# Kernel tuning notes

Hardware: AMD Instinct MI355X
Metric: run time of the kernel (lower is better)

Reference implementation:

```python
import jax, jax.numpy as jnp
import numpy as np

B, S, D = 4, 2048, 768

def setup_inputs() -> dict:
    key = jax.random.key(0)
    ks = jax.random.split(key, 7)
    scale = 1.0 / np.sqrt(D)
    x = jax.random.normal(ks[0], (B, S, D), dtype=jnp.float32)
    Wq = jax.random.uniform(ks[1], (D, D), jnp.float32, -scale, scale)
    bq = jax.random.uniform(ks[2], (D,), jnp.float32, -scale, scale)
    Wk = jax.random.uniform(ks[3], (D, D), jnp.float32, -scale, scale)
    bk = jax.random.uniform(ks[4], (D,), jnp.float32, -scale, scale)
    Wv = jax.random.uniform(ks[5], (D, D), jnp.float32, -scale, scale)
    bv = jax.random.uniform(ks[6], (D,), jnp.float32, -scale, scale)
    return {"x": x, "Wq": Wq, "bq": bq, "Wk": Wk, "bk": bk, "Wv": Wv, "bv": bv}

def reference(x, Wq, bq, Wk, bk, Wv, bv):
    d = x.shape[-1]
    q = jnp.einsum('bsd,de->bse', x, Wq) + bq
    k = jnp.einsum('bsd,de->bse', x, Wk) + bk
    v = jnp.einsum('bsd,de->bse', x, Wv) + bv
    scores = jnp.einsum('bqd,bkd->bqk', q, k) / jnp.sqrt(jnp.asarray(d, x.dtype))
    attn = jax.nn.softmax(scores, axis=-1)  # [B,S,S]
    return jnp.einsum('bqk,bkd->bqd', attn, v)
```

## Files before the change

kernel.cpp:

```cpp
#include <hip/hip_runtime.h>
#include <hip/hip_bf16.h>


typedef __attribute__((ext_vector_type(8))) short short8;
typedef __attribute__((ext_vector_type(4))) short short4v;
typedef __attribute__((ext_vector_type(4))) float float4v;

static constexpr int B_ = 4, S_ = 2048, D_ = 768;
static constexpr int MS = B_ * S_;

__device__ inline short f2bf(float f) {
  __hip_bfloat16 h = __float2bfloat16(f);
  union { __hip_bfloat16 h; short s; } u; u.h = h; return u.s;
}
__device__ inline float bf2f(short s) {
  union { unsigned int u; float f; } c;
  c.u = ((unsigned int)(unsigned short)s) << 16; return c.f;
}

typedef const __attribute__((address_space(1))) unsigned int g_u32;
typedef __attribute__((address_space(3))) unsigned int l_u32;

__device__ __forceinline__ void glds16(const short* g, short* l) {
  __builtin_amdgcn_global_load_lds((g_u32*)g, (l_u32*)l, 16, 0, 0);
}

__global__ __launch_bounds__(256)
void cast_f32_bf16(const float* __restrict__ x, short* __restrict__ y, int n) {
  int i = (blockIdx.x * 256 + threadIdx.x) * 4;
  if (i + 3 < n) {
    float4v v = *(const float4v*)(x + i);
    short4v o;
    o.x = f2bf(v.x); o.y = f2bf(v.y); o.z = f2bf(v.z); o.w = f2bf(v.w);
    *(short4v*)(y + i) = o;
  }
}

__global__ void transpose_cast_w(const float* __restrict__ W0, const float* __restrict__ W1,
                                 const float* __restrict__ W2,
                                 short* __restrict__ T0, short* __restrict__ T1,
                                 short* __restrict__ T2) {
  const float* W = blockIdx.z == 0 ? W0 : (blockIdx.z == 1 ? W1 : W2);
  short* T = blockIdx.z == 0 ? T0 : (blockIdx.z == 1 ? T1 : T2);
  __shared__ float tile[32][33];
  int bx = blockIdx.x * 32, by = blockIdx.y * 32;
  int tx = threadIdx.x, ty = threadIdx.y;
  for (int r = ty; r < 32; r += 8)
    tile[r][tx] = W[(by + r) * D_ + bx + tx];
  __syncthreads();
  for (int r = ty; r < 32; r += 8)
    T[(bx + r) * D_ + by + tx] = f2bf(tile[tx][r]);
}

template<int EPI, int TM, int TN>
__global__ __launch_bounds__(256)
void gemm_bt(const short* __restrict__ A, const short* __restrict__ Bt,
             void* __restrict__ C0v, short* __restrict__ C1, short* __restrict__ C2,
             const float* __restrict__ bias0, const float* __restrict__ bias1,
             const float* __restrict__ bias2,
             int K, int lda, int ldb, int ldc,
             long sA, long sB, long sC, float scale) {
  constexpr int BMv = TM * 32, BNv = TN * 32;
  const int b = blockIdx.z;
  A += (long)b * sA;
  Bt += (long)b * sB;
  float* Cf = (float*)C0v + (long)b * sC;
  short* Cs = (short*)C0v + (long)b * sC;

  __shared__ short As[BMv * 64];
  __shared__ short Bs[BNv * 64];

  const int t = threadIdx.x;
  const int wave = t >> 6, lane = t & 63;
  const int lane16 = lane & 15, q = lane >> 4;
  const int m0 = blockIdx.y * BMv, n0 = blockIdx.x * BNv;
  const int wm = (wave >> 1) * (TM * 16), wn = (wave & 1) * (TN * 16);
  const int rsub = lane >> 3;
  const int g = (lane & 7) ^ rsub;

  auto stage = [&](int kk) {
#pragma unroll
    for (int i = wave; i < BMv / 8; i += 4)
      glds16(A + (long)(m0 + i * 8 + rsub) * lda + kk + g * 8, &As[i * 512]);
#pragma unroll
    for (int i = wave; i < BNv / 8; i += 4)
      glds16(Bt + (long)(n0 + i * 8 + rsub) * ldb + kk + g * 8, &Bs[i * 512]);
  };

  stage(0);

  float4v acc[TM][TN];
#pragma unroll
  for (int i = 0; i < TM; i++)
#pragma unroll
    for (int j = 0; j < TN; j++) acc[i][j] = {0.f, 0.f, 0.f, 0.f};

  float4v acc_rs[TM];
#pragma unroll
  for (int i = 0; i < TM; i++) acc_rs[i] = {0.f, 0.f, 0.f, 0.f};
  short8 ones;
#pragma unroll
  for (int e = 0; e < 8; e++) ones[e] = (short)0x3F80;

  for (int k0 = 0; k0 < K; k0 += 64) {
    __syncthreads();

    short8 af[2][TM], bfr[2][TN];
#pragma unroll
    for (int s = 0; s < 2; s++) {
#pragma unroll
      for (int i = 0; i < TM; i++) {
        int R = wm + i * 16 + lane16;
        af[s][i] = *(const short8*)&As[R * 64 + (((s * 4 + q) ^ (R & 7)) * 8)];
      }
#pragma unroll
      for (int j = 0; j < TN; j++) {
        int R = wn + j * 16 + lane16;
        bfr[s][j] = *(const short8*)&Bs[R * 64 + (((s * 4 + q) ^ (R & 7)) * 8)];
      }
    }
    __syncthreads();

    if (k0 + 64 < K) stage(k0 + 64);

#pragma unroll
    for (int s = 0; s < 2; s++) {
#pragma unroll
      for (int i = 0; i < TM; i++) {
#pragma unroll
        for (int j = 0; j < TN; j++)
          acc[i][j] = __builtin_amdgcn_mfma_f32_16x16x32_bf16(af[s][i], bfr[s][j], acc[i][j], 0, 0, 0);
        if (EPI == 3)
          acc_rs[i] = __builtin_amdgcn_mfma_f32_16x16x32_bf16(af[s][i], ones, acc_rs[i], 0, 0, 0);
      }
    }
  }

#pragma unroll
  for (int i = 0; i < TM; i++) {
    int mrow = m0 + wm + i * 16 + q * 4;
    if (EPI == 0) {
#pragma unroll
      for (int j = 0; j < TN; j++) {
        int ncol = n0 + wn + j * 16 + lane16;
        if (ncol < 1536) {
          short* dst = ncol < 768 ? Cs : C1;
          const float* bs = ncol < 768 ? bias0 : bias1;
          int c = ncol < 768 ? ncol : ncol - 768;
#pragma unroll
          for (int rr = 0; rr < 4; rr++)
            dst[(long)(mrow + rr) * 768 + c] = f2bf(acc[i][j][rr] + bs[c]);
        } else {
          int e = ncol - 1536;
          float bv = bias2[e];
          short4v o;
#pragma unroll
          for (int rr = 0; rr < 4; rr++) o[rr] = f2bf(acc[i][j][rr] + bv);
          *(short4v*)&C2[(long)e * MS + mrow] = o;
        }
      }
    } else if (EPI == 2) {
#pragma unroll
      for (int j = 0; j < TN; j++) {
        int ncol = n0 + wn + j * 16 + lane16;
#pragma unroll
        for (int rr = 0; rr < 4; rr++)
          Cs[(long)(mrow + rr) * ldc + ncol] = f2bf(__expf(acc[i][j][rr] * scale));
      }
    } else {
#pragma unroll
      for (int rr = 0; rr < 4; rr++) {
        float inv = 1.0f / acc_rs[i][rr];
#pragma unroll
        for (int j = 0; j < TN; j++) {
          int ncol = n0 + wn + j * 16 + lane16;
          Cf[(long)(mrow + rr) * ldc + ncol] = acc[i][j][rr] * inv;
        }
      }
    }
  }
}

extern "C" void kernel_launch(void* const* d_in, const int* in_sizes, int n_in,
                              void* d_out, int out_size, void* d_ws, size_t ws_size,
                              hipStream_t stream) {
  const float* x  = (const float*)d_in[0];
  const float* Wq = (const float*)d_in[1];
  const float* bq = (const float*)d_in[2];
  const float* Wk = (const float*)d_in[3];
  const float* bk = (const float*)d_in[4];
  const float* Wv = (const float*)d_in[5];
  const float* bv = (const float*)d_in[6];
  float* out = (float*)d_out;

  short* Xb  = (short*)d_ws;
  short* WqT = Xb + (long)MS * D_;
  short* WkT = WqT + (long)D_ * D_;
  short* WvT = WkT + (long)D_ * D_;
  short* Qb  = WvT + (long)D_ * D_;
  short* Kb  = Qb + (long)MS * D_;
  short* Vt  = Kb + (long)MS * D_;
  short* Es  = Vt + (long)MS * D_;

  cast_f32_bf16<<<(MS * D_) / 1024, 256, 0, stream>>>(x, Xb, MS * D_);
  transpose_cast_w<<<dim3(24, 24, 3), dim3(32, 8), 0, stream>>>(Wq, Wk, Wv, WqT, WkT, WvT);

  gemm_bt<0, 4, 4><<<dim3(2304 / 128, MS / 128, 1), 256, 0, stream>>>(
      Xb, WqT, Qb, Kb, Vt, bq, bk, bv,
      D_, D_, D_, D_, 0, 0, 0, 1.0f);
  gemm_bt<2, 4, 4><<<dim3(S_ / 128, S_ / 128, B_), 256, 0, stream>>>(
      Qb, Kb, Es, nullptr, nullptr, nullptr, nullptr, nullptr,
      D_, D_, D_, S_,
      (long)S_ * D_, (long)S_ * D_, (long)S_ * S_, 1.0f / sqrtf((float)D_));
  gemm_bt<3, 4, 4><<<dim3(D_ / 128, S_ / 128, B_), 256, 0, stream>>>(
      Es, Vt, out, nullptr, nullptr, nullptr, nullptr, nullptr,
      S_, S_, MS, D_,
      (long)S_ * S_, (long)S_, (long)S_ * D_, 1.0f);
}
```

Measured before the change: 203.7 us.

## Add 256x256 eight-wave pipelined GEMM for QKV projection and scores

Adds a new GEMM kernel that uses 256x256 tiles, 512 threads and double-buffered LDS. Global-to-LDS loads are staged in quarter-tile pieces and interleaved with four MFMA phases, using explicit barriers, waitcnt and setprio. The QKV projection and the QK^T exp kernels switch to it, while the PV kernel stays on the old path. The larger tiles improve data reuse and hide memory latency, at the cost of 128KB of LDS per block, fewer blocks per CU and heavier register pressure.

```diff
diff --git a/kernel.cpp b/kernel.cpp
--- a/kernel.cpp
+++ b/kernel.cpp
@@ -12,10 +12,6 @@
 __device__ inline short f2bf(float f) {
   __hip_bfloat16 h = __float2bfloat16(f);
   union { __hip_bfloat16 h; short s; } u; u.h = h; return u.s;
-}
-__device__ inline float bf2f(short s) {
-  union { unsigned int u; float f; } c;
-  c.u = ((unsigned int)(unsigned short)s) << 16; return c.f;
 }
 
 typedef const __attribute__((address_space(1))) unsigned int g_u32;
@@ -181,6 +177,194 @@
   }
 }
 
+template<int EPI>
+__global__ __launch_bounds__(512, 2)
+void gemm8p(const short* __restrict__ A, const short* __restrict__ Bt,
+            void* __restrict__ C0v, short* __restrict__ C1, short* __restrict__ C2,
+            const float* __restrict__ bias0, const float* __restrict__ bias1,
+            const float* __restrict__ bias2,
+            int K, int lda, int ldb, int ldc,
+            long sA, long sB, long sC, float scale) {
+  const int b = blockIdx.z;
+  A += (long)b * sA;
+  Bt += (long)b * sB;
+  short* Cs = (short*)C0v + (long)b * sC;
+
+  __shared__ short As[2][256 * 64];
+  __shared__ short Bs[2][256 * 64];
+
+  const int t = threadIdx.x;
+  const int wave = t >> 6, lane = t & 63;
+  const int lane16 = lane & 15, q = lane >> 4;
+  const int xr = lane16 & 7;
+  const int m0 = blockIdx.y * 256, n0 = blockIdx.x * 256;
+  const int wm = (wave >> 2) * 128, wn = (wave & 3) * 64;
+  const int rsub = lane >> 3;
+  const int g = (lane & 7) ^ rsub;
+  const int nt = K >> 6;
+
+  auto stageA = [&](int u, int tt) {
+    short* dst = &As[tt & 1][0];
+    const short* src = A + tt * 64 + g * 8;
+#pragma unroll
+    for (int r = 0; r < 2; r++) {
+      int row0 = u * 64 + r * 128 + wave * 8;
+      glds16(src + (long)(m0 + row0 + rsub) * lda, dst + row0 * 64);
+    }
+  };
+  auto stageB = [&](int u, int tt) {
+    short* dst = &Bs[tt & 1][0];
+    const short* src = Bt + tt * 64 + g * 8;
+#pragma unroll
+    for (int r = 0; r < 2; r++) {
+      int idx = r * 8 + wave;
+      int row0 = (idx >> 2) * 64 + u * 32 + (idx & 3) * 8;
+      glds16(src + (long)(n0 + row0 + rsub) * ldb, dst + row0 * 64);
+    }
+  };
+
+  float4v acc[8][4];
+#pragma unroll
+  for (int i = 0; i < 8; i++)
+#pragma unroll
+    for (int j = 0; j < 4; j++) acc[i][j] = {0.f, 0.f, 0.f, 0.f};
+
+  stageA(0, 0); stageA(1, 0); stageB(0, 0); stageB(1, 0);
+  if (nt > 1) { stageA(0, 1); stageB(0, 1); stageA(1, 1); }
+  if (nt > 1) asm volatile("s_waitcnt vmcnt(6)" ::: "memory");
+  else        asm volatile("s_waitcnt vmcnt(0)" ::: "memory");
+  __builtin_amdgcn_s_barrier();
+
+#pragma unroll 2
+  for (int tt = 0; tt < nt; ++tt) {
+    const short* Ab = &As[tt & 1][0];
+    const short* Bb = &Bs[tt & 1][0];
+    short8 a[4][2], b0[2][2], b1[2][2];
+
+#pragma unroll
+    for (int ii = 0; ii < 4; ii++) {
+      int R = wm + ii * 16 + lane16;
+#pragma unroll
+      for (int s = 0; s < 2; s++)
+        a[ii][s] = *(const short8*)&Ab[R * 64 + (((s * 4 + q) ^ xr) * 8)];
+    }
+#pragma unroll
+    for (int jj = 0; jj < 2; jj++) {
+      int R = wn + jj * 16 + lane16;
+#pragma unroll
+      for (int s = 0; s < 2; s++)
+        b0[jj][s] = *(const short8*)&Bb[R * 64 + (((s * 4 + q) ^ xr) * 8)];
+    }
+    if (tt + 1 < nt) stageB(1, tt + 1);
+    __builtin_amdgcn_s_barrier();
+    asm volatile("s_waitcnt lgkmcnt(0)" ::: "memory");
+    __builtin_amdgcn_sched_barrier(0);
+    __builtin_amdgcn_s_setprio(1);
+#pragma unroll
+    for (int s = 0; s < 2; s++)
+#pragma unroll
+      for (int ii = 0; ii < 4; ii++)
+#pragma unroll
+        for (int jj = 0; jj < 2; jj++)
+          acc[ii][jj] = __builtin_amdgcn_mfma_f32_16x16x32_bf16(a[ii][s], b0[jj][s], acc[ii][jj], 0, 0, 0);
+    __builtin_amdgcn_s_setprio(0);
+    __builtin_amdgcn_s_barrier();
+
+#pragma unroll
+    for (int jj = 0; jj < 2; jj++) {
+      int R = wn + 32 + jj * 16 + lane16;
+#pragma unroll
+      for (int s = 0; s < 2; s++)
+        b1[jj][s] = *(const short8*)&Bb[R * 64 + (((s * 4 + q) ^ xr) * 8)];
+    }
+    if (tt + 2 < nt) stageA(0, tt + 2);
+    __builtin_amdgcn_s_barrier();
+    asm volatile("s_waitcnt lgkmcnt(0)" ::: "memory");
+    __builtin_amdgcn_sched_barrier(0);
+    __builtin_amdgcn_s_setprio(1);
+#pragma unroll
+    for (int s = 0; s < 2; s++)
+#pragma unroll
+      for (int ii = 0; ii < 4; ii++)
+#pragma unroll
+        for (int jj = 0; jj < 2; jj++)
+          acc[ii][2 + jj] = __builtin_amdgcn_mfma_f32_16x16x32_bf16(a[ii][s], b1[jj][s], acc[ii][2 + jj], 0, 0, 0);
+    __builtin_amdgcn_s_setprio(0);
+    __builtin_amdgcn_s_barrier();
+
+#pragma unroll
+    for (int ii = 0; ii < 4; ii++) {
+      int R = wm + 64 + ii * 16 + lane16;
+#pragma unroll
+      for (int s = 0; s < 2; s++)
+        a[ii][s] = *(const short8*)&Ab[R * 64 + (((s * 4 + q) ^ xr) * 8)];
+    }
+    if (tt + 2 < nt) stageB(0, tt + 2);
+    __builtin_amdgcn_s_barrier();
+    asm volatile("s_waitcnt lgkmcnt(0)" ::: "memory");
+    __builtin_amdgcn_sched_barrier(0);
+    __builtin_amdgcn_s_setprio(1);
+#pragma unroll
+    for (int s = 0; s < 2; s++)
+#pragma unroll
+      for (int ii = 0; ii < 4; ii++)
+#pragma unroll
+        for (int jj = 0; jj < 2; jj++)
+          acc[4 + ii][2 + jj] = __builtin_amdgcn_mfma_f32_16x16x32_bf16(a[ii][s], b1[jj][s], acc[4 + ii][2 + jj], 0, 0, 0);
+    __builtin_amdgcn_s_setprio(0);
+    __builtin_amdgcn_s_barrier();
+
+    if (tt + 2 < nt) stageA(1, tt + 2);
+    __builtin_amdgcn_s_barrier();
+    __builtin_amdgcn_s_setprio(1);
+#pragma unroll
+    for (int s = 0; s < 2; s++)
+#pragma unroll
+      for (int ii = 0; ii < 4; ii++)
+#pragma unroll
+        for (int jj = 0; jj < 2; jj++)
+          acc[4 + ii][jj] = __builtin_amdgcn_mfma_f32_16x16x32_bf16(a[ii][s], b0[jj][s], acc[4 + ii][jj], 0, 0, 0);
+    __builtin_amdgcn_s_setprio(0);
+    if (tt + 2 < nt) asm volatile("s_waitcnt vmcnt(6)" ::: "memory");
+    else             asm volatile("s_waitcnt vmcnt(0)" ::: "memory");
+    __builtin_amdgcn_s_barrier();
+  }
+
+#pragma unroll
+  for (int i = 0; i < 8; i++) {
+    int mrow = m0 + wm + i * 16 + q * 4;
+    if (EPI == 0) {
+#pragma unroll
+      for (int j = 0; j < 4; j++) {
+        int ncol = n0 + wn + j * 16 + lane16;
+        if (ncol < 1536) {
+          short* dst = ncol < 768 ? Cs : C1;
+          const float* bs = ncol < 768 ? bias0 : bias1;
+          int c = ncol < 768 ? ncol : ncol - 768;
+#pragma unroll
+          for (int rr = 0; rr < 4; rr++)
+            dst[(long)(mrow + rr) * 768 + c] = f2bf(acc[i][j][rr] + bs[c]);
+        } else {
+          int e = ncol - 1536;
+          float bv = bias2[e];
+          short4v o;
+#pragma unroll
+          for (int rr = 0; rr < 4; rr++) o[rr] = f2bf(acc[i][j][rr] + bv);
+          *(short4v*)&C2[(long)e * MS + mrow] = o;
+        }
+      }
+    } else {
+#pragma unroll
+      for (int j = 0; j < 4; j++) {
+        int ncol = n0 + wn + j * 16 + lane16;
+#pragma unroll
+        for (int rr = 0; rr < 4; rr++)
+          Cs[(long)(mrow + rr) * ldc + ncol] = f2bf(__expf(acc[i][j][rr] * scale));
+      }
+    }
+  }
+}
+
 extern "C" void kernel_launch(void* const* d_in, const int* in_sizes, int n_in,
                               void* d_out, int out_size, void* d_ws, size_t ws_size,
                               hipStream_t stream) {
@@ -205,10 +389,10 @@
   cast_f32_bf16<<<(MS * D_) / 1024, 256, 0, stream>>>(x, Xb, MS * D_);
   transpose_cast_w<<<dim3(24, 24, 3), dim3(32, 8), 0, stream>>>(Wq, Wk, Wv, WqT, WkT, WvT);
 
-  gemm_bt<0, 4, 4><<<dim3(2304 / 128, MS / 128, 1), 256, 0, stream>>>(
+  gemm8p<0><<<dim3(2304 / 256, MS / 256, 1), 512, 0, stream>>>(
       Xb, WqT, Qb, Kb, Vt, bq, bk, bv,
       D_, D_, D_, D_, 0, 0, 0, 1.0f);
-  gemm_bt<2, 4, 4><<<dim3(S_ / 128, S_ / 128, B_), 256, 0, stream>>>(
+  gemm8p<2><<<dim3(S_ / 256, S_ / 256, B_), 512, 0, stream>>>(
       Qb, Kb, Es, nullptr, nullptr, nullptr, nullptr, nullptr,
       D_, D_, D_, S_,
       (long)S_ * D_, (long)S_ * D_, (long)S_ * S_, 1.0f / sqrtf((float)D_));
```

After: 222.2 us. 1.09x slower.

## Fuse QK^T, exp and PV into a single attention kernel and merge prep kernels

Applied to the files above, without the earlier changes.

Replaces the separate score GEMM (which wrote exp(scores) as bf16 to a B*S*S buffer) and the PV GEMM with one fused attention kernel. Each block keeps a 32-row Q tile in LDS, streams K and V from global memory, computes exp scores into a small LDS tile and accumulates both the output and the row sums, normalizing at the end. This removes the large score-matrix round trip through HBM. The cast and weight-transpose prep kernels are merged into one launch, and an XCD-aware block swizzle is added to the projection GEMM. Risks: only 256 blocks of 512 threads, K and V are read straight from global memory without LDS staging, and there is still no max subtraction before the exponential.

```diff
diff --git a/kernel.cpp b/kernel.cpp
--- a/kernel.cpp
+++ b/kernel.cpp
@@ -13,10 +13,6 @@
   __hip_bfloat16 h = __float2bfloat16(f);
   union { __hip_bfloat16 h; short s; } u; u.h = h; return u.s;
 }
-__device__ inline float bf2f(short s) {
-  union { unsigned int u; float f; } c;
-  c.u = ((unsigned int)(unsigned short)s) << 16; return c.f;
-}
 
 typedef const __attribute__((address_space(1))) unsigned int g_u32;
 typedef __attribute__((address_space(3))) unsigned int l_u32;
@@ -25,47 +21,52 @@
   __builtin_amdgcn_global_load_lds((g_u32*)g, (l_u32*)l, 16, 0, 0);
 }
 
+__device__ __forceinline__ void xcd_swizzle(int& bx, int& by) {
+  const int gx = gridDim.x, nxy = gx * gridDim.y;
+  const int oid = blockIdx.y * gx + blockIdx.x;
+  const int nid = (oid & 7) * (nxy >> 3) + (oid >> 3);
+  bx = nid % gx;
+  by = nid / gx;
+}
+
 __global__ __launch_bounds__(256)
-void cast_f32_bf16(const float* __restrict__ x, short* __restrict__ y, int n) {
-  int i = (blockIdx.x * 256 + threadIdx.x) * 4;
-  if (i + 3 < n) {
+void prep(const float* __restrict__ x, short* __restrict__ Xb,
+          const float* __restrict__ W0, const float* __restrict__ W1,
+          const float* __restrict__ W2,
+          short* __restrict__ T0, short* __restrict__ T1, short* __restrict__ T2) {
+  __shared__ float tile[32][33];
+  const int t = threadIdx.x;
+  if (blockIdx.z == 0) {
+    int i = (blockIdx.x * 256 + t) * 4;
     float4v v = *(const float4v*)(x + i);
     short4v o;
     o.x = f2bf(v.x); o.y = f2bf(v.y); o.z = f2bf(v.z); o.w = f2bf(v.w);
-    *(short4v*)(y + i) = o;
-  }
-}
-
-__global__ void transpose_cast_w(const float* __restrict__ W0, const float* __restrict__ W1,
-                                 const float* __restrict__ W2,
-                                 short* __restrict__ T0, short* __restrict__ T1,
-                                 short* __restrict__ T2) {
-  const float* W = blockIdx.z == 0 ? W0 : (blockIdx.z == 1 ? W1 : W2);
-  short* T = blockIdx.z == 0 ? T0 : (blockIdx.z == 1 ? T1 : T2);
-  __shared__ float tile[32][33];
-  int bx = blockIdx.x * 32, by = blockIdx.y * 32;
-  int tx = threadIdx.x, ty = threadIdx.y;
-  for (int r = ty; r < 32; r += 8)
-    tile[r][tx] = W[(by + r) * D_ + bx + tx];
-  __syncthreads();
-  for (int r = ty; r < 32; r += 8)
-    T[(bx + r) * D_ + by + tx] = f2bf(tile[tx][r]);
-}
-
-template<int EPI, int TM, int TN>
+    *(short4v*)(Xb + i) = o;
+  } else {
+    int wid = blockIdx.x;
+    if (wid >= 1728) return;
+    int wz = wid / 576, rem = wid - wz * 576;
+    int wy = rem / 24, wx = rem - wy * 24;
+    const float* W = wz == 0 ? W0 : (wz == 1 ? W1 : W2);
+    short* T = wz == 0 ? T0 : (wz == 1 ? T1 : T2);
+    int bx = wx * 32, by = wy * 32;
+    int tx = t & 31, ty = t >> 5;
+    for (int r = ty; r < 32; r += 8)
+      tile[r][tx] = W[(by + r) * D_ + bx + tx];
+    __syncthreads();
+    for (int r = ty; r < 32; r += 8)
+      T[(bx + r) * D_ + by + tx] = f2bf(tile[tx][r]);
+  }
+}
+
+template<int TM, int TN>
 __global__ __launch_bounds__(256)
 void gemm_bt(const short* __restrict__ A, const short* __restrict__ Bt,
-             void* __restrict__ C0v, short* __restrict__ C1, short* __restrict__ C2,
+             short* __restrict__ C0, short* __restrict__ C1, short* __restrict__ C2,
              const float* __restrict__ bias0, const float* __restrict__ bias1,
              const float* __restrict__ bias2,
-             int K, int lda, int ldb, int ldc,
-             long sA, long sB, long sC, float scale) {
+             int K, int lda, int ldb) {
   constexpr int BMv = TM * 32, BNv = TN * 32;
-  const int b = blockIdx.z;
-  A += (long)b * sA;
-  Bt += (long)b * sB;
-  float* Cf = (float*)C0v + (long)b * sC;
-  short* Cs = (short*)C0v + (long)b * sC;
 
   __shared__ short As[BMv * 64];
   __shared__ short Bs[BNv * 64];
@@ -73,7 +74,9 @@
   const int t = threadIdx.x;
   const int wave = t >> 6, lane = t & 63;
   const int lane16 = lane & 15, q = lane >> 4;
-  const int m0 = blockIdx.y * BMv, n0 = blockIdx.x * BNv;
+  int bxs, bys;
+  xcd_swizzle(bxs, bys);
+  const int m0 = bys * BMv, n0 = bxs * BNv;
   const int wm = (wave >> 1) * (TM * 16), wn = (wave & 1) * (TN * 16);
   const int rsub = lane >> 3;
   const int g = (lane & 7) ^ rsub;
@@ -95,13 +98,6 @@
 #pragma unroll
     for (int j = 0; j < TN; j++) acc[i][j] = {0.f, 0.f, 0.f, 0.f};
 
-  float4v acc_rs[TM];
-#pragma unroll
-  for (int i = 0; i < TM; i++) acc_rs[i] = {0.f, 0.f, 0.f, 0.f};
-  short8 ones;
-#pragma unroll
-  for (int e = 0; e < 8; e++) ones[e] = (short)0x3F80;
-
   for (int k0 = 0; k0 < K; k0 += 64) {
     __syncthreads();
 
@@ -124,59 +120,155 @@
     if (k0 + 64 < K) stage(k0 + 64);
 
 #pragma unroll
-    for (int s = 0; s < 2; s++) {
-#pragma unroll
-      for (int i = 0; i < TM; i++) {
+    for (int s = 0; s < 2; s++)
+#pragma unroll
+      for (int i = 0; i < TM; i++)
 #pragma unroll
         for (int j = 0; j < TN; j++)
           acc[i][j] = __builtin_amdgcn_mfma_f32_16x16x32_bf16(af[s][i], bfr[s][j], acc[i][j], 0, 0, 0);
-        if (EPI == 3)
-          acc_rs[i] = __builtin_amdgcn_mfma_f32_16x16x32_bf16(af[s][i], ones, acc_rs[i], 0, 0, 0);
-      }
-    }
   }
 
 #pragma unroll
   for (int i = 0; i < TM; i++) {
     int mrow = m0 + wm + i * 16 + q * 4;
-    if (EPI == 0) {
-#pragma unroll
-      for (int j = 0; j < TN; j++) {
-        int ncol = n0 + wn + j * 16 + lane16;
-        if (ncol < 1536) {
-          short* dst = ncol < 768 ? Cs : C1;
-          const float* bs = ncol < 768 ? bias0 : bias1;
-          int c = ncol < 768 ? ncol : ncol - 768;
-#pragma unroll
-          for (int rr = 0; rr < 4; rr++)
-            dst[(long)(mrow + rr) * 768 + c] = f2bf(acc[i][j][rr] + bs[c]);
-        } else {
-          int e = ncol - 1536;
-          float bv = bias2[e];
-          short4v o;
-#pragma unroll
-          for (int rr = 0; rr < 4; rr++) o[rr] = f2bf(acc[i][j][rr] + bv);
-          *(short4v*)&C2[(long)e * MS + mrow] = o;
-        }
-      }
-    } else if (EPI == 2) {
-#pragma unroll
-      for (int j = 0; j < TN; j++) {
-        int ncol = n0 + wn + j * 16 + lane16;
+#pragma unroll
+    for (int j = 0; j < TN; j++) {
+      int ncol = n0 + wn + j * 16 + lane16;
+      if (ncol < 1536) {
+        short* dst = ncol < 768 ? C0 : C1;
+        const float* bs = ncol < 768 ? bias0 : bias1;
+        int c = ncol < 768 ? ncol : ncol - 768;
 #pragma unroll
         for (int rr = 0; rr < 4; rr++)
-          Cs[(long)(mrow + rr) * ldc + ncol] = f2bf(__expf(acc[i][j][rr] * scale));
-      }
-    } else {
+          dst[(long)(mrow + rr) * 768 + c] = f2bf(acc[i][j][rr] + bs[c]);
+      } else {
+        int e = ncol - 1536;
+        float bv = bias2[e];
+        short4v o;
+#pragma unroll
+        for (int rr = 0; rr < 4; rr++) o[rr] = f2bf(acc[i][j][rr] + bv);
+        *(short4v*)&C2[(long)e * MS + mrow] = o;
+      }
+    }
+  }
+}
+
+__global__ __launch_bounds__(512, 2)
+void fused_attn(const short* __restrict__ Qb, const short* __restrict__ Kb,
+                const short* __restrict__ Vt, float* __restrict__ out,
+                float scale) {
+  const int x = blockIdx.x;
+  const int xcd = x & 7, k = x >> 3;
+  const int b = xcd >> 1;
+  const int q0 = ((k << 1) | (xcd & 1)) * 32;
+
+  __shared__ short Qs[32 * 776];
+  __shared__ short Ps[32 * 128];
+  __shared__ float Rs[32];
+
+  const int t = threadIdx.x;
+  const int wave = t >> 6, lane = t & 63;
+  const int lane16 = lane & 15, q = lane >> 4;
+
+  {
+    const short* src = Qb + ((long)b * 2048 + q0) * 768;
+#pragma unroll
+    for (int i = 0; i < 6; i++) {
+      int g = i * 512 + t;
+      int row = g / 96, c = g - row * 96;
+      *(short8*)&Qs[row * 776 + c * 8] = *(const short8*)&src[(long)row * 768 + c * 8];
+    }
+  }
+  __syncthreads();
+
+  float4v acc_o[2][6];
+#pragma unroll
+  for (int m = 0; m < 2; m++)
+#pragma unroll
+    for (int n = 0; n < 6; n++) acc_o[m][n] = {0.f, 0.f, 0.f, 0.f};
+  float4v acc_rs[2];
+  acc_rs[0] = {0.f, 0.f, 0.f, 0.f};
+  acc_rs[1] = {0.f, 0.f, 0.f, 0.f};
+  short8 ones;
+#pragma unroll
+  for (int e = 0; e < 8; e++) ones[e] = (short)0x3F80;
+
+  const short* kbase = Kb + ((long)(b * 2048 + wave * 16 + lane16)) * 768 + q * 8;
+  const short* vbase = Vt + (long)b * 2048 + q * 8;
+
+  for (int kv0 = 0; kv0 < 2048; kv0 += 128) {
+    float4v s0 = {0.f, 0.f, 0.f, 0.f}, s1 = {0.f, 0.f, 0.f, 0.f};
+    const short* kr = kbase + (long)kv0 * 768;
+#pragma unroll 6
+    for (int kk = 0; kk < 768; kk += 32) {
+      short8 bf = *(const short8*)(kr + kk);
+      short8 a0 = *(const short8*)&Qs[lane16 * 776 + kk + q * 8];
+      short8 a1 = *(const short8*)&Qs[(16 + lane16) * 776 + kk + q * 8];
+      s0 = __builtin_amdgcn_mfma_f32_16x16x32_bf16(a0, bf, s0, 0, 0, 0);
+      s1 = __builtin_amdgcn_mfma_f32_16x16x32_bf16(a1, bf, s1, 0, 0, 0);
+    }
+
+    __syncthreads();
+
+#pragma unroll
+    for (int m = 0; m < 2; m++) {
+      float4v sv = m == 0 ? s0 : s1;
 #pragma unroll
       for (int rr = 0; rr < 4; rr++) {
-        float inv = 1.0f / acc_rs[i][rr];
-#pragma unroll
-        for (int j = 0; j < TN; j++) {
-          int ncol = n0 + wn + j * 16 + lane16;
-          Cf[(long)(mrow + rr) * ldc + ncol] = acc[i][j][rr] * inv;
-        }
-      }
+        int row = m * 16 + q * 4 + rr;
+        int c = wave * 16 + lane16;
+        int chunk = (c >> 3) ^ (row & 7);
+        Ps[row * 128 + chunk * 8 + (c & 7)] = f2bf(__expf(sv[rr] * scale));
+      }
+    }
+    __syncthreads();
+
+#pragma unroll
+    for (int kvk = 0; kvk < 4; kvk++) {
+      short8 pa[2];
+#pragma unroll
+      for (int m = 0; m < 2; m++) {
+        int row = m * 16 + lane16;
+        int c0 = kvk * 32 + q * 8;
+        int chunk = (c0 >> 3) ^ (row & 7);
+        pa[m] = *(const short8*)&Ps[row * 128 + chunk * 8];
+      }
+      if (wave == 0) {
+        acc_rs[0] = __builtin_amdgcn_mfma_f32_16x16x32_bf16(pa[0], ones, acc_rs[0], 0, 0, 0);
+        acc_rs[1] = __builtin_amdgcn_mfma_f32_16x16x32_bf16(pa[1], ones, acc_rs[1], 0, 0, 0);
+      }
+      const short* vr = vbase + kv0 + kvk * 32;
+#pragma unroll
+      for (int n = 0; n < 6; n++) {
+        int e = wave * 96 + n * 16 + lane16;
+        short8 vf = *(const short8*)(vr + (long)e * 8192);
+        acc_o[0][n] = __builtin_amdgcn_mfma_f32_16x16x32_bf16(pa[0], vf, acc_o[0][n], 0, 0, 0);
+        acc_o[1][n] = __builtin_amdgcn_mfma_f32_16x16x32_bf16(pa[1], vf, acc_o[1][n], 0, 0, 0);
+      }
+    }
+  }
+
+  if (wave == 0 && lane16 == 0) {
+#pragma unroll
+    for (int m = 0; m < 2; m++)
+#pragma unroll
+      for (int rr = 0; rr < 4; rr++)
+        Rs[m * 16 + q * 4 + rr] = acc_rs[m][rr];
+  }
+  __syncthreads();
+
+  float* ob = out + ((long)b * 2048 + q0) * 768;
+#pragma unroll
+  for (int m = 0; m < 2; m++) {
+    float rinv[4];
+#pragma unroll
+    for (int rr = 0; rr < 4; rr++) rinv[rr] = 1.0f / Rs[m * 16 + q * 4 + rr];
+#pragma unroll
+    for (int n = 0; n < 6; n++) {
+      int e = wave * 96 + n * 16 + lane16;
+#pragma unroll
+      for (int rr = 0; rr < 4; rr++)
+        ob[(long)(m * 16 + q * 4 + rr) * 768 + e] = acc_o[m][n][rr] * rinv[rr];
     }
   }
 }
@@ -200,20 +292,12 @@
   short* Qb  = WvT + (long)D_ * D_;
   short* Kb  = Qb + (long)MS * D_;
   short* Vt  = Kb + (long)MS * D_;
-  short* Es  = Vt + (long)MS * D_;
-
-  cast_f32_bf16<<<(MS * D_) / 1024, 256, 0, stream>>>(x, Xb, MS * D_);
-  transpose_cast_w<<<dim3(24, 24, 3), dim3(32, 8), 0, stream>>>(Wq, Wk, Wv, WqT, WkT, WvT);
-
-  gemm_bt<0, 4, 4><<<dim3(2304 / 128, MS / 128, 1), 256, 0, stream>>>(
-      Xb, WqT, Qb, Kb, Vt, bq, bk, bv,
-      D_, D_, D_, D_, 0, 0, 0, 1.0f);
-  gemm_bt<2, 4, 4><<<dim3(S_ / 128, S_ / 128, B_), 256, 0, stream>>>(
-      Qb, Kb, Es, nullptr, nullptr, nullptr, nullptr, nullptr,
-      D_, D_, D_, S_,
-      (long)S_ * D_, (long)S_ * D_, (long)S_ * S_, 1.0f / sqrtf((float)D_));
-  gemm_bt<3, 4, 4><<<dim3(D_ / 128, S_ / 128, B_), 256, 0, stream>>>(
-      Es, Vt, out, nullptr, nullptr, nullptr, nullptr, nullptr,
-      S_, S_, MS, D_,
-      (long)S_ * S_, (long)S_, (long)S_ * D_, 1.0f);
-}
+
+  prep<<<dim3(6144, 1, 2), 256, 0, stream>>>(x, Xb, Wq, Wk, Wv, WqT, WkT, WvT);
+
+  gemm_bt<4, 4><<<dim3(2304 / 128, MS / 128, 1), 256, 0, stream>>>(
+      Xb, WqT, Qb, Kb, Vt, bq, bk, bv, D_, D_, D_);
+
+  fused_attn<<<dim3(256, 1, 1), 512, 0, stream>>>(
+      Qb, Kb, Vt, out, 1.0f / sqrtf((float)D_));
+}
```

Result: slower. 305.9 us (+50.2%).
